# Optimization experiments

Measured on AMD Instinct MI355X. Metric: run time of the kernel, lower is better.

The kernel has to match this reference:

```python
import jax, jax.numpy as jnp
import numpy as np

N = 1024   # state dimension
L = 16384  # sequence length


def setup_inputs() -> dict:
    key = jax.random.key(0)
    k_u, k_a, k_b, k_c = jax.random.split(key, 4)
    u = jax.random.normal(k_u, (L,), dtype=jnp.float32)
    # lecun_normal: std = 1/sqrt(fan_in). Shift A by -I so the discretized
    # transition matrix Ab has spectral radius < 1 (otherwise Ab^L overflows).
    A = jax.random.normal(k_a, (N, N), dtype=jnp.float32) / np.sqrt(N) - jnp.eye(N, dtype=jnp.float32)
    B = jax.random.normal(k_b, (N, 1), dtype=jnp.float32) / np.sqrt(1.0)
    C = jax.random.normal(k_c, (1, N), dtype=jnp.float32) / np.sqrt(N)
    log_step = jnp.full((1, 1), np.log(0.01), dtype=jnp.float32)
    return {"u": u, "A": A, "B": B, "C": C, "log_step": log_step}


def reference(u, A, B, C, log_step):
    # --- discretize (bilinear / Tustin transform) ---
    step = jnp.exp(log_step)[0, 0]
    I = jnp.eye(A.shape[0], dtype=A.dtype)
    BL = jnp.linalg.inv(I - (step / 2.0) * A)
    Ab = BL @ (I + (step / 2.0) * A)     # (N, N)
    Bb = (step * BL) @ B                  # (N, 1)
    Cb = C                                # (1, N)

    # --- naive_kernel: K[l] = Cb @ Ab^l @ Bb, built as a scan recurrence ---
    def body(x, _):
        k_l = (Cb @ x)[0, 0]
        return Ab @ x, k_l

    _, K = jax.lax.scan(body, Bb, None, length=u.shape[0])  # (L,)

    # --- causal convolution: y[t] = sum_{l<=t} K[l] * u[t-l] ---
    y = jnp.convolve(u, K)[: u.shape[0]]
    return y
```

## Files before the change

### kernel.cpp

```cpp
#include <hip/hip_runtime.h>
#include <hip/hip_bf16.h>
#include <math.h>

#define N_DIM 1024
#define L_SEQ 16384

typedef unsigned short ushort_t;
typedef __bf16 bf16x8 __attribute__((ext_vector_type(8)));
typedef float f32x4 __attribute__((ext_vector_type(4)));

#define FW_F32 1
#define FW_SPLIT 2
#define FW_TSPLIT 4
#define FW_ADDD 8
#define FW_MKAB 16
#define FW_TPRE 32

#define AS1 __attribute__((address_space(1)))
#define AS3 __attribute__((address_space(3)))

__device__ __forceinline__ void split2(float v, ushort_t& h, ushort_t& m) {
  union { __bf16 b; ushort_t u; } c;
  __bf16 bh = (__bf16)v;
  float fh = (float)bh;
  c.b = bh; h = c.u;
  c.b = (__bf16)(v - fh); m = c.u;
}

__global__ __launch_bounds__(256) void k_scalesplit(const float* __restrict__ A,
    const float* __restrict__ ls, float* __restrict__ E,
    ushort_t* __restrict__ set) {
  const size_t NN = (size_t)N_DIM * N_DIM;
  float hs = 0.5f * expf(ls[0]);
  int t = threadIdx.x;
  int r0 = blockIdx.x * 64 + ((t >> 4) << 2);
  int c0 = blockIdx.y * 64 + ((t & 15) << 2);
  float v[4][4];
#pragma unroll
  for (int i = 0; i < 4; ++i) {
    float4 f = *(const float4*)&A[(size_t)(r0 + i) * N_DIM + c0];
    v[i][0] = hs * f.x; v[i][1] = hs * f.y; v[i][2] = hs * f.z; v[i][3] = hs * f.w;
    *(float4*)&E[(size_t)(r0 + i) * N_DIM + c0] =
        make_float4(v[i][0], v[i][1], v[i][2], v[i][3]);
  }
  ushort_t h[4][4], m[4][4];
#pragma unroll
  for (int i = 0; i < 4; ++i)
#pragma unroll
    for (int j = 0; j < 4; ++j) split2(v[i][j], h[i][j], m[i][j]);
#pragma unroll
  for (int i = 0; i < 4; ++i) {
    size_t o = (size_t)(r0 + i) * N_DIM + c0;
    *(ushort4*)&set[o] = make_ushort4(h[i][0], h[i][1], h[i][2], h[i][3]);
    *(ushort4*)&set[NN + o] = make_ushort4(m[i][0], m[i][1], m[i][2], m[i][3]);
  }
#pragma unroll
  for (int j = 0; j < 4; ++j) {
    size_t o = (size_t)(c0 + j) * N_DIM + r0;
    *(ushort4*)&set[2 * NN + o] = make_ushort4(h[0][j], h[1][j], h[2][j], h[3][j]);
    *(ushort4*)&set[3 * NN + o] = make_ushort4(m[0][j], m[1][j], m[2][j], m[3][j]);
  }
}

__global__ __launch_bounds__(256) void k_bbinit(ushort_t* __restrict__ VTset,
    ushort_t* __restrict__ Wset, const float* __restrict__ S,
    const float* __restrict__ B, const float* __restrict__ Cm,
    const float* __restrict__ ls) {
  const size_t KR = (size_t)128 * N_DIM;
  int bx = blockIdx.x;
  if (bx >= 256) {
    int i = (bx - 256) * 256 + threadIdx.x;
    ushort_t h, m; split2(Cm[i], h, m);
    Wset[i] = h; Wset[KR + i] = m;
    return;
  }
  int row = bx * 4 + (threadIdx.x >> 6);
  int lane = threadIdx.x & 63;
  const float* Sr = S + (size_t)row * N_DIM;
  float sum = 0.f;
  for (int k = lane; k < N_DIM; k += 64) sum += Sr[k] * B[k];
  for (int off = 32; off; off >>= 1) sum += __shfl_down(sum, off);
  if (lane == 0) {
    float step = expf(ls[0]);
    float bb = step * (B[row] + sum);
    ushort_t h, m; split2(bb, h, m);
    VTset[row] = h; VTset[KR + row] = m;
  }
}

__device__ __forceinline__ void skinny_q(
    ushort_t* lds, const ushort_t* __restrict__ SkB, ushort_t* __restrict__ Ka,
    int srcOff, int dstOff, int cnt, int id, int t) {
  const size_t NN = (size_t)N_DIM * N_DIM;
  const size_t KR = (size_t)128 * N_DIM;
  int rt = id >> 6, c16 = id & 63;
  if (rt * 16 >= cnt) return;
  const int lane = t & 63, w = t >> 6;
  const ushort_t* Ah = Ka;
  const ushort_t* Amm = Ka + KR;
  const ushort_t* Bh = SkB;
  const ushort_t* Bm = SkB + NN;

  auto stq = [&](int buf, int k0) {
    ushort_t* base = lds + buf * 2048;
    if (t < 128) {
      int pl = t >> 6, rem = t & 63, kc = rem >> 4, row = rem & 15;
      const ushort_t* src = (pl ? Amm : Ah) +
          (size_t)(srcOff + rt * 16 + row) * N_DIM + k0 + kc * 8;
      __builtin_amdgcn_global_load_lds((const AS1 void*)src,
                                       (AS3 void*)(base + t * 8), 16, 0, 0);
    } else {
      int t2 = t - 128;
      int pl = t2 >> 6, rem = t2 & 63, kc = rem >> 4, row = rem & 15;
      const ushort_t* src = (pl ? Bm : Bh) +
          (size_t)(c16 * 16 + row) * N_DIM + k0 + kc * 8;
      __builtin_amdgcn_global_load_lds((const AS1 void*)src,
                                       (AS3 void*)(base + 1024 + t2 * 8), 16, 0, 0);
    }
  };

  f32x4 acc = (f32x4){0.f, 0.f, 0.f, 0.f};
  const int lrow = lane & 15, kg = lane >> 4;

  stq(0, 0);
  stq(1, 32);
  for (int ks = 0; ks < 32; ++ks) {
    int cur = ks % 3;
    if (ks < 30) {
      stq((ks + 2) % 3, (ks + 2) * 32);
      asm volatile("s_waitcnt vmcnt(2)" ::: "memory");
    } else if (ks == 30) {
      asm volatile("s_waitcnt vmcnt(1)" ::: "memory");
    } else {
      asm volatile("s_waitcnt vmcnt(0)" ::: "memory");
    }
    __builtin_amdgcn_s_barrier();
    __builtin_amdgcn_sched_barrier(0);
    if (w == 0) {
      const ushort_t* b = lds + cur * 2048;
      bf16x8 a0 = *(const bf16x8*)&b[kg * 128 + lrow * 8];
      bf16x8 a1 = *(const bf16x8*)&b[512 + kg * 128 + lrow * 8];
      bf16x8 b0 = *(const bf16x8*)&b[1024 + kg * 128 + lrow * 8];
      bf16x8 b1 = *(const bf16x8*)&b[1536 + kg * 128 + lrow * 8];
      acc = __builtin_amdgcn_mfma_f32_16x16x32_bf16(a0, b0, acc, 0, 0, 0);
      acc = __builtin_amdgcn_mfma_f32_16x16x32_bf16(a0, b1, acc, 0, 0, 0);
      acc = __builtin_amdgcn_mfma_f32_16x16x32_bf16(a1, b0, acc, 0, 0, 0);
      acc = __builtin_amdgcn_mfma_f32_16x16x32_bf16(a1, b1, acc, 0, 0, 0);
    }
    if (ks < 31) __builtin_amdgcn_s_barrier();
  }

  if (w == 0) {
    int col = c16 * 16 + lrow;
#pragma unroll
    for (int j = 0; j < 4; ++j) {
      int irl = kg * 4 + j;
      if (rt * 16 + irl < cnt) {
        ushort_t h, m; split2(acc[j], h, m);
        Ka[(size_t)(dstOff + rt * 16 + irl) * N_DIM + col] = h;
        Ka[KR + (size_t)(dstOff + rt * 16 + irl) * N_DIM + col] = m;
      }
    }
  }
}

__global__ __launch_bounds__(256) void gemm4f(
    const ushort_t* __restrict__ Qa, const ushort_t* __restrict__ Qbt,
    const float* __restrict__ D, float* __restrict__ Cf,
    ushort_t* __restrict__ Oset, ushort_t* __restrict__ Oset2, int flags,
    const ushort_t* __restrict__ SkB, ushort_t* __restrict__ Ka,
    int srcOff, int dstOff, int cnt, int mode) {
  const size_t NN = (size_t)N_DIM * N_DIM;
  __shared__ __align__(16) ushort_t lds[32768];
  int t = threadIdx.x;
  const int lane = t & 63, w = t >> 6;
  int id = (int)blockIdx.y * 16 + (int)blockIdx.x;

  if (mode == 2) {
    skinny_q(lds, SkB, Ka, srcOff, dstOff, cnt, id, t);
    return;
  }

  {
    int m0 = blockIdx.x * 64, n0 = blockIdx.y * 64;
    int r = t & 63, kc = t >> 6;
    const ushort_t* gA[2] = {Qa, Qa + NN};
    const ushort_t* gB[2] = {Qbt, Qbt + NN};
    size_t aoff = (size_t)(m0 + r) * N_DIM + kc * 8;
    size_t boff = (size_t)(n0 + r) * N_DIM + kc * 8;

    auto stage = [&](int buf, int k0) {
      ushort_t* dst = lds + buf * 8192;
#pragma unroll
      for (int L = 0; L < 2; ++L) {
        __builtin_amdgcn_global_load_lds(
            (const AS1 void*)(gA[L] + aoff + k0),
            (AS3 void*)(dst + L * 2048 + t * 8), 16, 0, 0);
        __builtin_amdgcn_global_load_lds(
            (const AS1 void*)(gB[L] + boff + k0),
            (AS3 void*)(dst + 4096 + L * 2048 + t * 8), 16, 0, 0);
      }
    };

    f32x4 acc[2][2];
#pragma unroll
    for (int i = 0; i < 2; ++i)
#pragma unroll
      for (int j = 0; j < 2; ++j) acc[i][j] = (f32x4){0.f, 0.f, 0.f, 0.f};

    const int wm = (w >> 1) * 32, wn = (w & 1) * 32;
    const int lrow = lane & 15, kg = lane >> 4;
    const int aIdx0 = kg * 512 + (wm + lrow) * 8;
    const int bIdx0 = 4096 + kg * 512 + (wn + lrow) * 8;

    stage(0, 0);
    stage(1, 32);
    stage(2, 64);
    for (int ks = 0; ks < 32; ++ks) {
      int cur = ks & 3;
      if (ks < 29) {
        stage((ks + 3) & 3, (ks + 3) * 32);
        asm volatile("s_waitcnt vmcnt(12)" ::: "memory");
      } else if (ks == 29) {
        asm volatile("s_waitcnt vmcnt(8)" ::: "memory");
      } else if (ks == 30) {
        asm volatile("s_waitcnt vmcnt(4)" ::: "memory");
      } else {
        asm volatile("s_waitcnt vmcnt(0)" ::: "memory");
      }
      __builtin_amdgcn_s_barrier();
      __builtin_amdgcn_sched_barrier(0);
      const ushort_t* buf = lds + cur * 8192;
      bf16x8 a[2][2], b[2][2];
#pragma unroll
      for (int L = 0; L < 2; ++L) {
#pragma unroll
        for (int mi = 0; mi < 2; ++mi)
          a[L][mi] = *(const bf16x8*)&buf[L * 2048 + aIdx0 + mi * 128];
#pragma unroll
        for (int ni = 0; ni < 2; ++ni)
          b[L][ni] = *(const bf16x8*)&buf[bIdx0 + L * 2048 + ni * 128];
      }
#pragma unroll
      for (int mi = 0; mi < 2; ++mi)
#pragma unroll
        for (int ni = 0; ni < 2; ++ni) {
          f32x4 c = acc[mi][ni];
          c = __builtin_amdgcn_mfma_f32_16x16x32_bf16(a[0][mi], b[0][ni], c, 0, 0, 0);
          c = __builtin_amdgcn_mfma_f32_16x16x32_bf16(a[0][mi], b[1][ni], c, 0, 0, 0);
          c = __builtin_amdgcn_mfma_f32_16x16x32_bf16(a[1][mi], b[0][ni], c, 0, 0, 0);
          c = __builtin_amdgcn_mfma_f32_16x16x32_bf16(a[1][mi], b[1][ni], c, 0, 0, 0);
          acc[mi][ni] = c;
        }
      if (ks < 31) __builtin_amdgcn_s_barrier();
    }

#pragma unroll
    for (int mi = 0; mi < 2; ++mi)
#pragma unroll
      for (int ni = 0; ni < 2; ++ni) {
        int rowb = m0 + wm + mi * 16 + kg * 4;
        int col = n0 + wn + ni * 16 + lrow;
        float vv[4];
#pragma unroll
        for (int j = 0; j < 4; ++j) vv[j] = acc[mi][ni][j];
        if (flags & FW_TPRE) {
          ushort_t h[4], m[4];
#pragma unroll
          for (int j = 0; j < 4; ++j) split2(vv[j], h[j], m[j]);
          size_t o = (size_t)col * N_DIM + rowb;
          *(ushort4*)&Oset2[2 * NN + o] = make_ushort4(h[0], h[1], h[2], h[3]);
          *(ushort4*)&Oset2[3 * NN + o] = make_ushort4(m[0], m[1], m[2], m[3]);
        }
        if (flags & FW_ADDD) {
#pragma unroll
          for (int j = 0; j < 4; ++j) vv[j] += D[(size_t)(rowb + j) * N_DIM + col];
        }
        if (flags & FW_F32) {
#pragma unroll
          for (int j = 0; j < 4; ++j) Cf[(size_t)(rowb + j) * N_DIM + col] = vv[j];
        }
        if (flags & FW_MKAB) {
#pragma unroll
          for (int j = 0; j < 4; ++j)
            vv[j] = 2.0f * vv[j] + ((rowb + j) == col ? 1.0f : 0.0f);
        }
        if (flags & (FW_SPLIT | FW_TSPLIT)) {
          ushort_t h[4], m[4];
#pragma unroll
          for (int j = 0; j < 4; ++j) split2(vv[j], h[j], m[j]);
          if (flags & FW_SPLIT) {
#pragma unroll
            for (int j = 0; j < 4; ++j) {
              size_t o = (size_t)(rowb + j) * N_DIM + col;
              Oset[o] = h[j]; Oset[NN + o] = m[j];
            }
          }
          if (flags & FW_TSPLIT) {
            size_t o = (size_t)col * N_DIM + rowb;
            *(ushort4*)&Oset[2 * NN + o] = make_ushort4(h[0], h[1], h[2], h[3]);
            *(ushort4*)&Oset[3 * NN + o] = make_ushort4(m[0], m[1], m[2], m[3]);
          }
        }
      }
  }

  if (mode == 1) {
    __syncthreads();
    skinny_q(lds, SkB, Ka, srcOff, dstOff, cnt, id, t);
  }
}

__global__ __launch_bounds__(256) void k_combine(
    const ushort_t* __restrict__ Wset, const ushort_t* __restrict__ Vset,
    float* __restrict__ Kv) {
  const size_t KR = (size_t)128 * N_DIM;
  __shared__ __align__(16) ushort_t lds[15360];
  int t = threadIdx.x;
  int rt = blockIdx.x, ct = blockIdx.y;
  const ushort_t* Ah = Wset;
  const ushort_t* Amm = Wset + KR;
  const ushort_t* Bh = Vset;
  const ushort_t* Bm = Vset + KR;
  const int lane = t & 63, w = t >> 6;
  const int lrow = lane & 15, kg = lane >> 4;

  auto stageS = [&](int buf, int k0) {
    ushort_t* base = lds + buf * 5120;
    if (t < 128) {
      int lvl = t >> 6, rem = t & 63, kcc = rem >> 4, i = rem & 15;
      const ushort_t* src =
          (lvl ? Amm : Ah) + (size_t)(rt * 16 + i) * N_DIM + k0 + kcc * 8;
      __builtin_amdgcn_global_load_lds((const AS1 void*)src,
                                       (AS3 void*)(base + t * 8), 16, 0, 0);
    }
#pragma unroll
    for (int it = 0; it < 2; ++it) {
      int t2 = t + it * 256;
      int lvl = t2 >> 8, rem = t2 & 255, kcc = rem >> 6, c = rem & 63;
      const ushort_t* src =
          (lvl ? Bm : Bh) + (size_t)(ct * 64 + c) * N_DIM + k0 + kcc * 8;
      __builtin_amdgcn_global_load_lds(
          (const AS1 void*)src, (AS3 void*)(base + 1024 + t2 * 8), 16, 0, 0);
    }
  };

  f32x4 acc = (f32x4){0.f, 0.f, 0.f, 0.f};
  const int aO = kg * 128 + lrow * 8;
  const int bO = 1024 + kg * 512 + (w * 16 + lrow) * 8;

  stageS(0, 0);
  stageS(1, 32);
  for (int ks = 0; ks < 32; ++ks) {
    int cur = ks % 3;
    if (ks < 30) {
      stageS((ks + 2) % 3, (ks + 2) * 32);
      if (w < 2) asm volatile("s_waitcnt vmcnt(6)" ::: "memory");
      else       asm volatile("s_waitcnt vmcnt(4)" ::: "memory");
    } else if (ks == 30) {
      if (w < 2) asm volatile("s_waitcnt vmcnt(3)" ::: "memory");
      else       asm volatile("s_waitcnt vmcnt(2)" ::: "memory");
    } else {
      asm volatile("s_waitcnt vmcnt(0)" ::: "memory");
    }
    __builtin_amdgcn_s_barrier();
    __builtin_amdgcn_sched_barrier(0);
    const ushort_t* b = lds + cur * 5120;
    bf16x8 a0 = *(const bf16x8*)&b[aO];
    bf16x8 a1 = *(const bf16x8*)&b[aO + 512];
    bf16x8 b0v = *(const bf16x8*)&b[bO];
    bf16x8 b1v = *(const bf16x8*)&b[bO + 2048];
    acc = __builtin_amdgcn_mfma_f32_16x16x32_bf16(a0, b0v, acc, 0, 0, 0);
    acc = __builtin_amdgcn_mfma_f32_16x16x32_bf16(a0, b1v, acc, 0, 0, 0);
    acc = __builtin_amdgcn_mfma_f32_16x16x32_bf16(a1, b0v, acc, 0, 0, 0);
    acc = __builtin_amdgcn_mfma_f32_16x16x32_bf16(a1, b1v, acc, 0, 0, 0);
    if (ks < 31) __builtin_amdgcn_s_barrier();
  }

  int rcol = ct * 64 + w * 16 + lrow;
#pragma unroll
  for (int j = 0; j < 4; ++j) {
    int q = rt * 16 + kg * 4 + j;
    Kv[q * 128 + rcol] = acc[j];
  }
}

__global__ __launch_bounds__(256) void conv_k(const float* __restrict__ Kv,
    const float* __restrict__ u, float* __restrict__ y) {
  const int CT = 1024, CJ = 256, LCH = 1024;
  int t0 = blockIdx.x * CT;
  int l0 = blockIdx.y * LCH;
  if (l0 > t0 + CT - 1) return;
  __shared__ __align__(16) float Ks[CJ];
  __shared__ __align__(16) float us[CT + CJ + 8];
  int tid = threadIdx.x;
  float acc0 = 0.f, acc1 = 0.f, acc2 = 0.f, acc3 = 0.f;
  int ltEnd = l0 + LCH; if (ltEnd > t0 + CT) ltEnd = t0 + CT;
  for (int lt = l0; lt < ltEnd; lt += CJ) {
    __syncthreads();
    Ks[tid] = Kv[lt + tid];
    int ub = t0 - lt - (CJ - 1);
    for (int s = tid; s < CT + CJ + 4; s += 256) {
      int g = ub + s;
      us[s] = (g >= 0 && g < L_SEQ) ? u[g] : 0.f;
    }
    __syncthreads();
    const float4* u4 = (const float4*)us;
    float4 wa = u4[tid];
#pragma unroll 4
    for (int jb = 0; jb < CJ / 4; ++jb) {
      float4 wb = u4[tid + jb + 1];
      float4 k4 = *(const float4*)&Ks[CJ - 4 - (jb << 2)];
      acc0 += k4.w * wa.x + k4.z * wa.y + k4.y * wa.z + k4.x * wa.w;
      acc1 += k4.w * wa.y + k4.z * wa.z + k4.y * wa.w + k4.x * wb.x;
      acc2 += k4.w * wa.z + k4.z * wa.w + k4.y * wb.x + k4.x * wb.y;
      acc3 += k4.w * wa.w + k4.z * wb.x + k4.y * wb.y + k4.x * wb.z;
      wa = wb;
    }
  }
  int t = t0 + (tid << 2);
  atomicAdd(&y[t + 0], acc0);
  atomicAdd(&y[t + 1], acc1);
  atomicAdd(&y[t + 2], acc2);
  atomicAdd(&y[t + 3], acc3);
}


extern "C" void kernel_launch(void* const* d_in, const int* in_sizes, int n_in,
                              void* d_out, int out_size, void* d_ws, size_t ws_size,
                              hipStream_t stream) {
  const float* u  = (const float*)d_in[0];
  const float* A  = (const float*)d_in[1];
  const float* B  = (const float*)d_in[2];
  const float* Cm = (const float*)d_in[3];
  const float* ls = (const float*)d_in[4];
  float* y  = (float*)d_out;
  float* ws = (float*)d_ws;

  const int N = N_DIM;
  const size_t NN = (size_t)N * N;
  const size_t KR = (size_t)128 * N;
  float* b0 = ws;
  float* b2 = b0 + NN;
  float* Kv = b2 + NN;
  ushort_t* setA = (ushort_t*)(Kv + L_SEQ);
  ushort_t* setB = setA + 4 * NN;
  ushort_t* setC = setB + 4 * NN;
  ushort_t* VTset = setC + 4 * NN;
  ushort_t* Wset = VTset + 2 * KR;

  hipMemsetAsync(y, 0, (size_t)L_SEQ * sizeof(float), stream);

  dim3 g16(16, 16);
  dim3 gQ32(16, 8);

  k_scalesplit<<<g16, 256, 0, stream>>>(A, ls, b0, setA);
  gemm4f<<<g16, 256, 0, stream>>>(setA, setA + 2 * NN, b0, b2, setC, setB,
                                  FW_TPRE | FW_ADDD | FW_F32 | FW_SPLIT,
                                  nullptr, nullptr, 0, 0, 0, 0);
  gemm4f<<<g16, 256, 0, stream>>>(setC, setB + 2 * NN, b2, b0, setA, nullptr,
                                  FW_ADDD | FW_F32 | FW_MKAB | FW_SPLIT | FW_TSPLIT,
                                  nullptr, nullptr, 0, 0, 0, 0);
  k_bbinit<<<260, 256, 0, stream>>>(VTset, Wset, b0, B, Cm, ls);

  ushort_t* cur = setA;
  ushort_t* oth = setB;
  for (int e = 0; e < 12; ++e) {
    int right = (e < 7);
    int s = 1 << (right ? e : (e - 7));
    ushort_t* Ka = right ? VTset : Wset;
    const ushort_t* SkB = right ? cur : cur + 2 * NN;
    int fl = (e == 11) ? FW_TSPLIT : (FW_SPLIT | FW_TSPLIT);
    gemm4f<<<g16, 256, 0, stream>>>(cur, cur + 2 * NN, nullptr, nullptr,
                                    oth, nullptr, fl, SkB, Ka, 0, s, s, 1);
    ushort_t* tmp = cur; cur = oth; oth = tmp;
  }
  const ushort_t* Q12T = cur + 2 * NN;
  for (int p = 0; p < 3; ++p)
    gemm4f<<<gQ32, 256, 0, stream>>>(cur, cur, nullptr, nullptr,
                                     nullptr, nullptr, 0, Q12T, Wset,
                                     32 * p, 32 + 32 * p, 32, 2);
  k_combine<<<dim3(8, 2), 256, 0, stream>>>(Wset, VTset, Kv);
  conv_k<<<g16, 256, 0, stream>>>(Kv, u, y);
}
```

Before: 414.1 us.

## Interleave skinny Krylov GEMM into main GEMM k-loop pipeline

The skinny Ka·SkB product used to run after the main 64x64 GEMM tile finished, as a separate skinny_q phase. It is now staged through an extra LDS region alongside the main tile loads, and wave 0 issues its four MFMAs inside each k-step. This is meant to hide the skinny product's loads and serial tail behind the main GEMM pipeline. In exchange LDS grows from 64KB to 80KB, which may lower occupancy, and wave 0 carries extra work that can unbalance the waves at each barrier.

```diff
diff --git a/kernel.cpp b/kernel.cpp
--- a/kernel.cpp
+++ b/kernel.cpp
@@ -171,7 +171,8 @@
     const ushort_t* __restrict__ SkB, ushort_t* __restrict__ Ka,
     int srcOff, int dstOff, int cnt, int mode) {
   const size_t NN = (size_t)N_DIM * N_DIM;
-  __shared__ __align__(16) ushort_t lds[32768];
+  const size_t KR = (size_t)128 * N_DIM;
+  __shared__ __align__(16) ushort_t lds[40960];
   int t = threadIdx.x;
   const int lane = t & 63, w = t >> 6;
   int id = (int)blockIdx.y * 16 + (int)blockIdx.x;
@@ -181,133 +182,184 @@
     return;
   }
 
-  {
-    int m0 = blockIdx.x * 64, n0 = blockIdx.y * 64;
-    int r = t & 63, kc = t >> 6;
-    const ushort_t* gA[2] = {Qa, Qa + NN};
-    const ushort_t* gB[2] = {Qbt, Qbt + NN};
-    size_t aoff = (size_t)(m0 + r) * N_DIM + kc * 8;
-    size_t boff = (size_t)(n0 + r) * N_DIM + kc * 8;
-
-    auto stage = [&](int buf, int k0) {
-      ushort_t* dst = lds + buf * 8192;
-#pragma unroll
-      for (int L = 0; L < 2; ++L) {
-        __builtin_amdgcn_global_load_lds(
-            (const AS1 void*)(gA[L] + aoff + k0),
-            (AS3 void*)(dst + L * 2048 + t * 8), 16, 0, 0);
-        __builtin_amdgcn_global_load_lds(
-            (const AS1 void*)(gB[L] + boff + k0),
-            (AS3 void*)(dst + 4096 + L * 2048 + t * 8), 16, 0, 0);
-      }
-    };
-
-    f32x4 acc[2][2];
-#pragma unroll
-    for (int i = 0; i < 2; ++i)
-#pragma unroll
-      for (int j = 0; j < 2; ++j) acc[i][j] = (f32x4){0.f, 0.f, 0.f, 0.f};
-
-    const int wm = (w >> 1) * 32, wn = (w & 1) * 32;
-    const int lrow = lane & 15, kg = lane >> 4;
-    const int aIdx0 = kg * 512 + (wm + lrow) * 8;
-    const int bIdx0 = 4096 + kg * 512 + (wn + lrow) * 8;
-
-    stage(0, 0);
-    stage(1, 32);
-    stage(2, 64);
-    for (int ks = 0; ks < 32; ++ks) {
-      int cur = ks & 3;
-      if (ks < 29) {
-        stage((ks + 3) & 3, (ks + 3) * 32);
+  int m0 = blockIdx.x * 64, n0 = blockIdx.y * 64;
+  int r = t & 63, kc = t >> 6;
+  const ushort_t* gA[2] = {Qa, Qa + NN};
+  const ushort_t* gB[2] = {Qbt, Qbt + NN};
+  size_t aoff = (size_t)(m0 + r) * N_DIM + kc * 8;
+  size_t boff = (size_t)(n0 + r) * N_DIM + kc * 8;
+
+  int rt = id >> 6, c16 = id & 63;
+  bool hasSk = (mode == 1) && (rt * 16 < cnt);
+  const ushort_t* skAh = Ka;
+  const ushort_t* skAm = Ka + KR;
+  const ushort_t* skBh = SkB;
+  const ushort_t* skBm = SkB ? SkB + NN : SkB;
+
+  auto stage = [&](int buf, int k0) {
+    ushort_t* dst = lds + buf * 8192;
+#pragma unroll
+    for (int L = 0; L < 2; ++L) {
+      __builtin_amdgcn_global_load_lds(
+          (const AS1 void*)(gA[L] + aoff + k0),
+          (AS3 void*)(dst + L * 2048 + t * 8), 16, 0, 0);
+      __builtin_amdgcn_global_load_lds(
+          (const AS1 void*)(gB[L] + boff + k0),
+          (AS3 void*)(dst + 4096 + L * 2048 + t * 8), 16, 0, 0);
+    }
+  };
+  auto stq = [&](int buf, int k0) {
+    ushort_t* base = lds + 32768 + buf * 2048;
+    if (t < 128) {
+      int pl = t >> 6, rem = t & 63, skc = rem >> 4, row = rem & 15;
+      const ushort_t* src = (pl ? skAm : skAh) +
+          (size_t)(srcOff + rt * 16 + row) * N_DIM + k0 + skc * 8;
+      __builtin_amdgcn_global_load_lds((const AS1 void*)src,
+                                       (AS3 void*)(base + t * 8), 16, 0, 0);
+    } else {
+      int t2 = t - 128;
+      int pl = t2 >> 6, rem = t2 & 63, skc = rem >> 4, row = rem & 15;
+      const ushort_t* src = (pl ? skBm : skBh) +
+          (size_t)(c16 * 16 + row) * N_DIM + k0 + skc * 8;
+      __builtin_amdgcn_global_load_lds((const AS1 void*)src,
+                                       (AS3 void*)(base + 1024 + t2 * 8), 16, 0, 0);
+    }
+  };
+
+  f32x4 acc[2][2];
+#pragma unroll
+  for (int i = 0; i < 2; ++i)
+#pragma unroll
+    for (int j = 0; j < 2; ++j) acc[i][j] = (f32x4){0.f, 0.f, 0.f, 0.f};
+  f32x4 skacc = (f32x4){0.f, 0.f, 0.f, 0.f};
+
+  const int wm = (w >> 1) * 32, wn = (w & 1) * 32;
+  const int lrow = lane & 15, kg = lane >> 4;
+  const int aIdx0 = kg * 512 + (wm + lrow) * 8;
+  const int bIdx0 = 4096 + kg * 512 + (wn + lrow) * 8;
+
+#pragma unroll
+  for (int p = 0; p < 3; ++p) {
+    stage(p, p * 32);
+    if (hasSk) stq(p, p * 32);
+  }
+  for (int ks = 0; ks < 32; ++ks) {
+    int cur = ks & 3;
+    if (ks < 29) {
+      stage((ks + 3) & 3, (ks + 3) * 32);
+      if (hasSk) {
+        stq((ks + 3) & 3, (ks + 3) * 32);
+        asm volatile("s_waitcnt vmcnt(15)" ::: "memory");
+      } else {
         asm volatile("s_waitcnt vmcnt(12)" ::: "memory");
-      } else if (ks == 29) {
-        asm volatile("s_waitcnt vmcnt(8)" ::: "memory");
-      } else if (ks == 30) {
-        asm volatile("s_waitcnt vmcnt(4)" ::: "memory");
-      } else {
-        asm volatile("s_waitcnt vmcnt(0)" ::: "memory");
-      }
-      __builtin_amdgcn_s_barrier();
-      __builtin_amdgcn_sched_barrier(0);
-      const ushort_t* buf = lds + cur * 8192;
-      bf16x8 a[2][2], b[2][2];
-#pragma unroll
-      for (int L = 0; L < 2; ++L) {
-#pragma unroll
-        for (int mi = 0; mi < 2; ++mi)
-          a[L][mi] = *(const bf16x8*)&buf[L * 2048 + aIdx0 + mi * 128];
-#pragma unroll
-        for (int ni = 0; ni < 2; ++ni)
-          b[L][ni] = *(const bf16x8*)&buf[bIdx0 + L * 2048 + ni * 128];
-      }
+      }
+    } else if (ks == 29) {
+      if (hasSk) asm volatile("s_waitcnt vmcnt(10)" ::: "memory");
+      else       asm volatile("s_waitcnt vmcnt(8)" ::: "memory");
+    } else if (ks == 30) {
+      if (hasSk) asm volatile("s_waitcnt vmcnt(5)" ::: "memory");
+      else       asm volatile("s_waitcnt vmcnt(4)" ::: "memory");
+    } else {
+      asm volatile("s_waitcnt vmcnt(0)" ::: "memory");
+    }
+    __builtin_amdgcn_s_barrier();
+    __builtin_amdgcn_sched_barrier(0);
+    const ushort_t* buf = lds + cur * 8192;
+    bf16x8 a[2][2], b[2][2];
+#pragma unroll
+    for (int L = 0; L < 2; ++L) {
 #pragma unroll
       for (int mi = 0; mi < 2; ++mi)
-#pragma unroll
-        for (int ni = 0; ni < 2; ++ni) {
-          f32x4 c = acc[mi][ni];
-          c = __builtin_amdgcn_mfma_f32_16x16x32_bf16(a[0][mi], b[0][ni], c, 0, 0, 0);
-          c = __builtin_amdgcn_mfma_f32_16x16x32_bf16(a[0][mi], b[1][ni], c, 0, 0, 0);
-          c = __builtin_amdgcn_mfma_f32_16x16x32_bf16(a[1][mi], b[0][ni], c, 0, 0, 0);
-          c = __builtin_amdgcn_mfma_f32_16x16x32_bf16(a[1][mi], b[1][ni], c, 0, 0, 0);
-          acc[mi][ni] = c;
-        }
-      if (ks < 31) __builtin_amdgcn_s_barrier();
-    }
-
+        a[L][mi] = *(const bf16x8*)&buf[L * 2048 + aIdx0 + mi * 128];
+#pragma unroll
+      for (int ni = 0; ni < 2; ++ni)
+        b[L][ni] = *(const bf16x8*)&buf[bIdx0 + L * 2048 + ni * 128];
+    }
 #pragma unroll
     for (int mi = 0; mi < 2; ++mi)
 #pragma unroll
       for (int ni = 0; ni < 2; ++ni) {
-        int rowb = m0 + wm + mi * 16 + kg * 4;
-        int col = n0 + wn + ni * 16 + lrow;
-        float vv[4];
-#pragma unroll
-        for (int j = 0; j < 4; ++j) vv[j] = acc[mi][ni][j];
-        if (flags & FW_TPRE) {
-          ushort_t h[4], m[4];
-#pragma unroll
-          for (int j = 0; j < 4; ++j) split2(vv[j], h[j], m[j]);
-          size_t o = (size_t)col * N_DIM + rowb;
-          *(ushort4*)&Oset2[2 * NN + o] = make_ushort4(h[0], h[1], h[2], h[3]);
-          *(ushort4*)&Oset2[3 * NN + o] = make_ushort4(m[0], m[1], m[2], m[3]);
-        }
-        if (flags & FW_ADDD) {
-#pragma unroll
-          for (int j = 0; j < 4; ++j) vv[j] += D[(size_t)(rowb + j) * N_DIM + col];
-        }
-        if (flags & FW_F32) {
-#pragma unroll
-          for (int j = 0; j < 4; ++j) Cf[(size_t)(rowb + j) * N_DIM + col] = vv[j];
-        }
-        if (flags & FW_MKAB) {
-#pragma unroll
-          for (int j = 0; j < 4; ++j)
-            vv[j] = 2.0f * vv[j] + ((rowb + j) == col ? 1.0f : 0.0f);
-        }
-        if (flags & (FW_SPLIT | FW_TSPLIT)) {
-          ushort_t h[4], m[4];
-#pragma unroll
-          for (int j = 0; j < 4; ++j) split2(vv[j], h[j], m[j]);
-          if (flags & FW_SPLIT) {
-#pragma unroll
-            for (int j = 0; j < 4; ++j) {
-              size_t o = (size_t)(rowb + j) * N_DIM + col;
-              Oset[o] = h[j]; Oset[NN + o] = m[j];
-            }
-          }
-          if (flags & FW_TSPLIT) {
-            size_t o = (size_t)col * N_DIM + rowb;
-            *(ushort4*)&Oset[2 * NN + o] = make_ushort4(h[0], h[1], h[2], h[3]);
-            *(ushort4*)&Oset[3 * NN + o] = make_ushort4(m[0], m[1], m[2], m[3]);
+        f32x4 c = acc[mi][ni];
+        c = __builtin_amdgcn_mfma_f32_16x16x32_bf16(a[0][mi], b[0][ni], c, 0, 0, 0);
+        c = __builtin_amdgcn_mfma_f32_16x16x32_bf16(a[0][mi], b[1][ni], c, 0, 0, 0);
+        c = __builtin_amdgcn_mfma_f32_16x16x32_bf16(a[1][mi], b[0][ni], c, 0, 0, 0);
+        c = __builtin_amdgcn_mfma_f32_16x16x32_bf16(a[1][mi], b[1][ni], c, 0, 0, 0);
+        acc[mi][ni] = c;
+      }
+    if (hasSk && w == 0) {
+      const ushort_t* sb = lds + 32768 + cur * 2048;
+      bf16x8 sa0 = *(const bf16x8*)&sb[kg * 128 + lrow * 8];
+      bf16x8 sa1 = *(const bf16x8*)&sb[512 + kg * 128 + lrow * 8];
+      bf16x8 sb0 = *(const bf16x8*)&sb[1024 + kg * 128 + lrow * 8];
+      bf16x8 sb1 = *(const bf16x8*)&sb[1536 + kg * 128 + lrow * 8];
+      skacc = __builtin_amdgcn_mfma_f32_16x16x32_bf16(sa0, sb0, skacc, 0, 0, 0);
+      skacc = __builtin_amdgcn_mfma_f32_16x16x32_bf16(sa0, sb1, skacc, 0, 0, 0);
+      skacc = __builtin_amdgcn_mfma_f32_16x16x32_bf16(sa1, sb0, skacc, 0, 0, 0);
+      skacc = __builtin_amdgcn_mfma_f32_16x16x32_bf16(sa1, sb1, skacc, 0, 0, 0);
+    }
+    if (ks < 31) __builtin_amdgcn_s_barrier();
+  }
+
+#pragma unroll
+  for (int mi = 0; mi < 2; ++mi)
+#pragma unroll
+    for (int ni = 0; ni < 2; ++ni) {
+      int rowb = m0 + wm + mi * 16 + kg * 4;
+      int col = n0 + wn + ni * 16 + lrow;
+      float vv[4];
+#pragma unroll
+      for (int j = 0; j < 4; ++j) vv[j] = acc[mi][ni][j];
+      if (flags & FW_TPRE) {
+        ushort_t h[4], m[4];
+#pragma unroll
+        for (int j = 0; j < 4; ++j) split2(vv[j], h[j], m[j]);
+        size_t o = (size_t)col * N_DIM + rowb;
+        *(ushort4*)&Oset2[2 * NN + o] = make_ushort4(h[0], h[1], h[2], h[3]);
+        *(ushort4*)&Oset2[3 * NN + o] = make_ushort4(m[0], m[1], m[2], m[3]);
+      }
+      if (flags & FW_ADDD) {
+#pragma unroll
+        for (int j = 0; j < 4; ++j) vv[j] += D[(size_t)(rowb + j) * N_DIM + col];
+      }
+      if (flags & FW_F32) {
+#pragma unroll
+        for (int j = 0; j < 4; ++j) Cf[(size_t)(rowb + j) * N_DIM + col] = vv[j];
+      }
+      if (flags & FW_MKAB) {
+#pragma unroll
+        for (int j = 0; j < 4; ++j)
+          vv[j] = 2.0f * vv[j] + ((rowb + j) == col ? 1.0f : 0.0f);
+      }
+      if (flags & (FW_SPLIT | FW_TSPLIT)) {
+        ushort_t h[4], m[4];
+#pragma unroll
+        for (int j = 0; j < 4; ++j) split2(vv[j], h[j], m[j]);
+        if (flags & FW_SPLIT) {
+#pragma unroll
+          for (int j = 0; j < 4; ++j) {
+            size_t o = (size_t)(rowb + j) * N_DIM + col;
+            Oset[o] = h[j]; Oset[NN + o] = m[j];
           }
         }
-      }
-  }
-
-  if (mode == 1) {
-    __syncthreads();
-    skinny_q(lds, SkB, Ka, srcOff, dstOff, cnt, id, t);
+        if (flags & FW_TSPLIT) {
+          size_t o = (size_t)col * N_DIM + rowb;
+          *(ushort4*)&Oset[2 * NN + o] = make_ushort4(h[0], h[1], h[2], h[3]);
+          *(ushort4*)&Oset[3 * NN + o] = make_ushort4(m[0], m[1], m[2], m[3]);
+        }
+      }
+    }
+
+  if (hasSk && w == 0) {
+    int col = c16 * 16 + lrow;
+#pragma unroll
+    for (int j = 0; j < 4; ++j) {
+      int irl = kg * 4 + j;
+      if (rt * 16 + irl < cnt) {
+        ushort_t h, m; split2(skacc[j], h, m);
+        Ka[(size_t)(dstOff + rt * 16 + irl) * N_DIM + col] = h;
+        Ka[KR + (size_t)(dstOff + rt * 16 + irl) * N_DIM + col] = m;
+      }
+    }
   }
 }
 
```

New measurement: 395.5 us. -4.5%, faster.
